# Optimization experiments

Measured on AMD Instinct MI355X. Metric: run time of the kernel, lower is better.

The kernel has to match this reference:

```python
import jax, jax.numpy as jnp
import numpy as np
import math

NUM_HEADS = 8
LN_EPS = 1e-8


def setup_inputs() -> dict:
    key = jax.random.key(0)
    ks = jax.random.split(key, 8)
    B, S, D = 16, 1024, 1024
    s = 1.0 / math.sqrt(D)
    return {
        "queries": jax.random.normal(ks[0], (B, S, D), dtype=jnp.float32),
        "keys": jax.random.normal(ks[1], (B, S, D), dtype=jnp.float32),
        "Wq": jax.random.normal(ks[2], (D, D), dtype=jnp.float32) * s,
        "bq": jnp.zeros((D,), dtype=jnp.float32),
        "Wk": jax.random.normal(ks[3], (D, D), dtype=jnp.float32) * s,
        "bk": jnp.zeros((D,), dtype=jnp.float32),
        "Wv": jax.random.normal(ks[4], (D, D), dtype=jnp.float32) * s,
        "bv": jnp.zeros((D,), dtype=jnp.float32),
        "ln_gamma": jnp.ones((D,), dtype=jnp.float32),
        "ln_beta": jnp.zeros((D,), dtype=jnp.float32),
    }


def _split_heads(x, H):
    # [B, S, D] -> [B*H, S, D/H], batch-major flattening (b*H + h), matching torch
    B, S, D = x.shape
    d = D // H
    return x.reshape(B, S, H, d).transpose(0, 2, 1, 3).reshape(B * H, S, d)


def _merge_heads(x, B, H):
    # [B*H, S, d] -> [B, S, H*d]
    BH, S, d = x.shape
    return x.reshape(B, H, S, d).transpose(0, 2, 1, 3).reshape(B, S, H * d)


def reference(queries, keys, Wq, bq, Wk, bk, Wv, bv, ln_gamma, ln_beta):
    B, S, D = queries.shape
    K_len = keys.shape[1]
    H = NUM_HEADS

    # ReLU'd QKV projections (nn.Linear uses x @ W.T + b)
    Q = jax.nn.relu(jnp.einsum("bsd,ed->bse", queries, Wq) + bq)
    K = jax.nn.relu(jnp.einsum("bsd,ed->bse", keys, Wk) + bk)
    V = jax.nn.relu(jnp.einsum("bsd,ed->bse", keys, Wv) + bv)

    Q_ = _split_heads(Q, H)  # [B*H, S, d]
    K_ = _split_heads(K, H)
    V_ = _split_heads(V, H)
    d_k = K_.shape[-1]

    scores = jnp.einsum("nsd,ntd->nst", Q_, K_) / jnp.sqrt(jnp.float32(d_k))
    attn = jax.nn.softmax(scores, axis=-1)  # [B*H, S, K_len]

    # post-softmax multiplicative mask: mask of nonzero query rows, tiled
    # head-major (mask.repeat(H,1,1)) exactly as the torch code does
    mask = (jnp.sum(jnp.abs(queries), axis=-1, keepdims=True) > 0).astype(queries.dtype)  # [B, S, 1]
    mask = jnp.broadcast_to(mask, (B, S, K_len))
    mask = jnp.tile(mask, (H, 1, 1))  # [H*B, S, K_len], index i -> batch i % B
    attn = attn * mask
    # dropout is identity in eval mode

    out = jnp.einsum("nst,ntd->nsd", attn, V_)  # [B*H, S, d]
    out = _merge_heads(out, B, H)  # [B, S, D]
    out = out + queries

    # LayerNorm over last dim, eps=1e-8
    mu = jnp.mean(out, axis=-1, keepdims=True)
    var = jnp.mean(jnp.square(out - mu), axis=-1, keepdims=True)
    out = (out - mu) / jnp.sqrt(var + LN_EPS) * ln_gamma + ln_beta
    return out
```

## Files before the change

### kernel.cpp

```cpp
#include <hip/hip_runtime.h>
#include <hip/hip_bf16.h>

#define B_ 16
#define S_ 1024
#define D_ 1024
#define H_ 8

typedef __attribute__((ext_vector_type(4))) float f32x4;
typedef __attribute__((ext_vector_type(8))) short s16x8;
typedef __attribute__((ext_vector_type(4))) short s16x4;
typedef unsigned int u32;

static __device__ __forceinline__ short f2bf(float x) {
  union { __hip_bfloat16 h; short s; } cv;
  cv.h = __float2bfloat16(x);
  return cv.s;
}
static __device__ __forceinline__ float bf2f(short x) {
  union { float f; u32 u; } cv;
  cv.u = ((u32)(unsigned short)x) << 16;
  return cv.f;
}
static __device__ __forceinline__ float exp2_hw(float x) {
  float r;
  asm("v_exp_f32 %0, %1" : "=v"(r) : "v"(x));
  return r;
}
static __device__ __forceinline__ void async16(const void* g, void* l) {
  __builtin_amdgcn_global_load_lds((const __attribute__((address_space(1))) u32*)g,
                                   (__attribute__((address_space(3))) u32*)l, 16, 0, 0);
}

#define QSCALE 0.12751741530f

__global__ __launch_bounds__(256) void cvt_qk(const float* __restrict__ q,
                                              const float* __restrict__ k,
                                              short* __restrict__ qb,
                                              short* __restrict__ kb) {
  int i = blockIdx.x * 256 + threadIdx.x;
  const float* s;
  short* d;
  int j;
  if (i < 2097152) { s = q; d = qb; j = i; }
  else             { s = k; d = kb; j = i - 2097152; }
  const float4* s4 = (const float4*)s;
  float4 a = s4[2 * j], b = s4[2 * j + 1];
  s16x8 r;
  r[0] = f2bf(a.x); r[1] = f2bf(a.y); r[2] = f2bf(a.z); r[3] = f2bf(a.w);
  r[4] = f2bf(b.x); r[5] = f2bf(b.y); r[6] = f2bf(b.z); r[7] = f2bf(b.w);
  *(s16x8*)(d + (size_t)j * 8) = r;
}

__global__ __launch_bounds__(256) void cvt_w(const float* __restrict__ wq,
                                             const float* __restrict__ wk,
                                             const float* __restrict__ wv,
                                             short* __restrict__ dq,
                                             short* __restrict__ dk,
                                             short* __restrict__ dv) {
  int i = blockIdx.x * 256 + threadIdx.x;
  const float* s;
  short* d;
  int j;
  if (i < 131072)      { s = wq; d = dq; j = i; }
  else if (i < 262144) { s = wk; d = dk; j = i - 131072; }
  else                 { s = wv; d = dv; j = i - 262144; }
  const float4* s4 = (const float4*)s;
  float4 a = s4[2 * j], b = s4[2 * j + 1];
  s16x8 r;
  r[0] = f2bf(a.x); r[1] = f2bf(a.y); r[2] = f2bf(a.z); r[3] = f2bf(a.w);
  r[4] = f2bf(b.x); r[5] = f2bf(b.y); r[6] = f2bf(b.z); r[7] = f2bf(b.w);
  *(s16x8*)(d + (size_t)j * 8) = r;
}

__global__ __launch_bounds__(256, 2) void gemm_qkv(
    const short* __restrict__ qb, const short* __restrict__ kb,
    const short* __restrict__ wq, const short* __restrict__ wk,
    const short* __restrict__ wv, const float* __restrict__ bq,
    const float* __restrict__ bk, const float* __restrict__ bv,
    short* __restrict__ Qb, short* __restrict__ Kb, short* __restrict__ Vb) {
  __shared__ short lA[128 * 64];
  __shared__ short lB[128 * 64];
  const short* A; const short* W; const float* bias; short* C;
  float scl;
  switch (blockIdx.z) {
    case 0:  A = qb; W = wq; bias = bq; C = Qb; scl = QSCALE; break;
    case 1:  A = kb; W = wk; bias = bk; C = Kb; scl = 1.f; break;
    default: A = kb; W = wv; bias = bv; C = Vb; scl = 1.f; break;
  }
  const int t = threadIdx.x;
  const int w = t >> 6, l = t & 63, lg = l >> 4, li = l & 15;
  const int wr = w >> 1, wc = w & 1;
  const int m0 = blockIdx.y << 7, n0 = blockIdx.x << 7;

  f32x4 acc[4][4];
#pragma unroll
  for (int m = 0; m < 4; ++m)
#pragma unroll
    for (int n = 0; n < 4; ++n) acc[m][n] = {0.f, 0.f, 0.f, 0.f};

  const char* Ab = (const char*)A + (size_t)m0 * 2048;
  const char* Wb = (const char*)W + (size_t)n0 * 2048;

#pragma unroll 1
  for (int k0 = 0; k0 < 1024; k0 += 64) {
    __syncthreads();
#pragma unroll
    for (int it = 0; it < 4; ++it) {
      int e = it * 256 + t;
      int row = e >> 3;
      int sb = ((e & 7) << 4) ^ ((row & 7) << 4);
      async16(Ab + (size_t)row * 2048 + k0 * 2 + sb, (char*)lA + e * 16);
      async16(Wb + (size_t)row * 2048 + k0 * 2 + sb, (char*)lB + e * 16);
    }
    __syncthreads();
#pragma unroll
    for (int kk = 0; kk < 2; ++kk) {
      s16x8 af[4], bfr[4];
#pragma unroll
      for (int m = 0; m < 4; ++m) {
        int row = wr * 64 + m * 16 + li;
        af[m] = *(const s16x8*)((char*)lA + row * 128 +
                                ((kk * 64 + (lg << 4)) ^ ((row & 7) << 4)));
      }
#pragma unroll
      for (int n = 0; n < 4; ++n) {
        int row = wc * 64 + n * 16 + li;
        bfr[n] = *(const s16x8*)((char*)lB + row * 128 +
                                 ((kk * 64 + (lg << 4)) ^ ((row & 7) << 4)));
      }
#pragma unroll
      for (int m = 0; m < 4; ++m)
#pragma unroll
        for (int n = 0; n < 4; ++n)
          acc[m][n] = __builtin_amdgcn_mfma_f32_16x16x32_bf16(af[m], bfr[n],
                                                              acc[m][n], 0, 0, 0);
    }
  }
#pragma unroll
  for (int n = 0; n < 4; ++n) {
    int col = n0 + wc * 64 + n * 16 + li;
    float bb = bias[col];
#pragma unroll
    for (int m = 0; m < 4; ++m) {
      int row0 = m0 + wr * 64 + m * 16 + (lg << 2);
#pragma unroll
      for (int r = 0; r < 4; ++r) {
        float v = acc[m][n][r] + bb;
        v = (v > 0.f ? v : 0.f) * scl;
        C[(size_t)(row0 + r) * 1024 + col] = f2bf(v);
      }
    }
  }
}

__global__ __launch_bounds__(256, 2) void attn_kernel(
    const short* __restrict__ Qb, const short* __restrict__ Kb,
    const short* __restrict__ Vb, short* __restrict__ Ob) {
  __shared__ short lK[64 * 128];
  __shared__ short lV[128 * 88];
  __shared__ short lP[128 * 64];

  const int t = threadIdx.x;
  const int w = t >> 6, l = t & 63, lg = l >> 4, li = l & 15;
  const int wgid = blockIdx.x;
  const int bh = ((wgid & 7) << 4) + (wgid >> 6);
  const int q0 = ((wgid >> 3) & 7) << 7;
  const int b = bh >> 3, h = bh & 7;
  const size_t hbase = (size_t)b * (S_ * D_) + h * 128;
  const short* Kh = Kb + hbase;
  const short* Vh = Vb + hbase;

  s16x8 qf[2][4];
#pragma unroll
  for (int m = 0; m < 2; ++m)
#pragma unroll
    for (int kk = 0; kk < 4; ++kk) {
      int row = q0 + (w << 5) + m * 16 + li;
      qf[m][kk] = *(const s16x8*)(Qb + hbase + (size_t)row * D_ + kk * 32 + (lg << 3));
    }

  f32x4 o[2][8];
#pragma unroll
  for (int m = 0; m < 2; ++m)
#pragma unroll
    for (int nd = 0; nd < 8; ++nd) o[m][nd] = {0.f, 0.f, 0.f, 0.f};
  float mrow[2][4], lrow[2][4];
#pragma unroll
  for (int m = 0; m < 2; ++m)
#pragma unroll
    for (int r = 0; r < 4; ++r) { mrow[m][r] = -1e30f; lrow[m][r] = 0.f; }

  s16x8 kreg[4], vr0[2], vr1[2];
#define LOADT(KT)                                                              \
  {                                                                            \
    _Pragma("unroll") for (int it = 0; it < 4; ++it) {                         \
      int e = it * 256 + t;                                                    \
      kreg[it] = *(const s16x8*)(Kh + (size_t)((KT)*64 + (e >> 4)) * 1024 +    \
                                 (e & 15) * 8);                                \
    }                                                                          \
    _Pragma("unroll") for (int vit = 0; vit < 2; ++vit) {                      \
      int e2 = vit * 256 + t;                                                  \
      int k0 = (e2 & 31) * 2, d0 = (e2 >> 5) * 8;                              \
      vr0[vit] = *(const s16x8*)(Vh + (size_t)((KT)*64 + k0) * 1024 + d0);     \
      vr1[vit] = *(const s16x8*)(Vh + (size_t)((KT)*64 + k0 + 1) * 1024 + d0); \
    }                                                                          \
  }

  LOADT(0);

#pragma unroll 1
  for (int kt = 0; kt < 16; ++kt) {
    __syncthreads();
#pragma unroll
    for (int it = 0; it < 4; ++it) {
      int e = it * 256 + t;
      int kr = e >> 4, kc = e & 15;
      *(s16x8*)((char*)lK + kr * 256 + ((kc * 16) ^ ((kr & 7) << 4))) = kreg[it];
    }
#pragma unroll
    for (int vit = 0; vit < 2; ++vit) {
      int e2 = vit * 256 + t;
      int k0 = (e2 & 31) * 2, d0 = (e2 >> 5) * 8;
#pragma unroll
      for (int j = 0; j < 8; ++j) {
        u32 pk = (u32)(unsigned short)vr0[vit][j] |
                 ((u32)(unsigned short)vr1[vit][j] << 16);
        *(u32*)((char*)lV + (d0 + j) * 176 + k0 * 2) = pk;
      }
    }
    __syncthreads();
    if (kt < 15) LOADT(kt + 1);

    f32x4 sc[2][4];
#pragma unroll
    for (int m = 0; m < 2; ++m)
#pragma unroll
      for (int n = 0; n < 4; ++n) sc[m][n] = {0.f, 0.f, 0.f, 0.f};
#pragma unroll
    for (int kk = 0; kk < 4; ++kk)
#pragma unroll
      for (int n = 0; n < 4; ++n) {
        int krow = n * 16 + li;
        s16x8 kf = *(const s16x8*)((char*)lK + krow * 256 +
                                   ((kk * 64 + (lg << 4)) ^ ((krow & 7) << 4)));
        sc[0][n] = __builtin_amdgcn_mfma_f32_16x16x32_bf16(qf[0][kk], kf, sc[0][n], 0, 0, 0);
        sc[1][n] = __builtin_amdgcn_mfma_f32_16x16x32_bf16(qf[1][kk], kf, sc[1][n], 0, 0, 0);
      }

    float tm[2][4];
    bool skip = true;
#pragma unroll
    for (int m = 0; m < 2; ++m)
#pragma unroll
      for (int r = 0; r < 4; ++r) {
        float v = fmaxf(fmaxf(sc[m][0][r], sc[m][1][r]),
                        fmaxf(sc[m][2][r], sc[m][3][r]));
        v = fmaxf(v, __shfl_xor(v, 1));
        v = fmaxf(v, __shfl_xor(v, 2));
        v = fmaxf(v, __shfl_xor(v, 4));
        v = fmaxf(v, __shfl_xor(v, 8));
        tm[m][r] = v;
        skip = skip && (v <= mrow[m][r] + 11.5f);
      }
    if (!__all(skip)) {
#pragma unroll
      for (int m = 0; m < 2; ++m)
#pragma unroll
        for (int r = 0; r < 4; ++r) {
          float mnew = fmaxf(mrow[m][r], tm[m][r]);
          float fsc = exp2_hw(mrow[m][r] - mnew);
          mrow[m][r] = mnew;
          lrow[m][r] *= fsc;
#pragma unroll
          for (int nd = 0; nd < 8; ++nd) o[m][nd][r] *= fsc;
        }
    }
#pragma unroll
    for (int m = 0; m < 2; ++m)
#pragma unroll
      for (int r = 0; r < 4; ++r) {
        float ps = 0.f;
#pragma unroll
        for (int n = 0; n < 4; ++n) {
          float p = exp2_hw(sc[m][n][r] - mrow[m][r]);
          sc[m][n][r] = p;
          ps += p;
        }
        ps += __shfl_xor(ps, 1);
        ps += __shfl_xor(ps, 2);
        ps += __shfl_xor(ps, 4);
        ps += __shfl_xor(ps, 8);
        lrow[m][r] += ps;
      }

#pragma unroll
    for (int m = 0; m < 2; ++m)
#pragma unroll
      for (int n = 0; n < 4; ++n)
#pragma unroll
        for (int r = 0; r < 4; ++r) {
          int prow = (w << 5) + m * 16 + (lg << 2) + r;
          int cb = ((n * 16 + li) << 1) ^ ((prow & 7) << 4);
          *(short*)((char*)lP + prow * 128 + cb) = f2bf(sc[m][n][r]);
        }
    asm volatile("s_waitcnt lgkmcnt(0)" ::: "memory");
    __builtin_amdgcn_sched_barrier(0);

#pragma unroll
    for (int ks = 0; ks < 2; ++ks) {
      int prow0 = (w << 5) + li;
      int prow1 = prow0 + 16;
      int kb3 = ks * 64 + (lg << 4);
      s16x8 pf0 = *(const s16x8*)((char*)lP + prow0 * 128 + (kb3 ^ ((prow0 & 7) << 4)));
      s16x8 pf1 = *(const s16x8*)((char*)lP + prow1 * 128 + (kb3 ^ ((prow1 & 7) << 4)));
#pragma unroll
      for (int nd = 0; nd < 8; ++nd) {
        int d = nd * 16 + li;
        s16x8 vf = *(const s16x8*)((char*)lV + d * 176 + kb3);
        o[0][nd] = __builtin_amdgcn_mfma_f32_16x16x32_bf16(pf0, vf, o[0][nd], 0, 0, 0);
        o[1][nd] = __builtin_amdgcn_mfma_f32_16x16x32_bf16(pf1, vf, o[1][nd], 0, 0, 0);
      }
    }
  }
#undef LOADT

#pragma unroll
  for (int m = 0; m < 2; ++m)
#pragma unroll
    for (int r = 0; r < 4; ++r) {
      float inv = 1.f / lrow[m][r];
      int row = q0 + (w << 5) + m * 16 + (lg << 2) + r;
      short* orow = Ob + hbase + (size_t)row * D_;
#pragma unroll
      for (int nd = 0; nd < 8; ++nd)
        orow[nd * 16 + li] = f2bf(o[m][nd][r] * inv);
    }
}

__global__ __launch_bounds__(256) void ln_ep(const float* __restrict__ q,
                                             const short* __restrict__ Ob,
                                             const float* __restrict__ gam,
                                             const float* __restrict__ bet,
                                             float* __restrict__ out) {
  __shared__ float red[4][8];
  const int t = threadIdx.x;
  const int w = t >> 6, l = t & 63;
  const size_t off = (size_t)blockIdx.x * 1024 + t * 4;
  float4 qv = *(const float4*)(q + off);
  s16x4 ov = *(const s16x4*)(Ob + off);
  float oa[4] = {bf2f(ov[0]), bf2f(ov[1]), bf2f(ov[2]), bf2f(ov[3])};
  float qa[4] = {qv.x, qv.y, qv.z, qv.w};
  float s0 = 0, s1 = 0, s2 = 0, s3 = 0, s4 = 0, s5 = 0;
#pragma unroll
  for (int j = 0; j < 4; ++j) {
    s0 += fabsf(qa[j]);
    s1 += oa[j];
    s2 += qa[j];
    s3 += oa[j] * oa[j];
    s4 += oa[j] * qa[j];
    s5 += qa[j] * qa[j];
  }
#pragma unroll
  for (int d2 = 1; d2 < 64; d2 <<= 1) {
    s0 += __shfl_xor(s0, d2); s1 += __shfl_xor(s1, d2); s2 += __shfl_xor(s2, d2);
    s3 += __shfl_xor(s3, d2); s4 += __shfl_xor(s4, d2); s5 += __shfl_xor(s5, d2);
  }
  if (l == 0) {
    red[w][0] = s0; red[w][1] = s1; red[w][2] = s2;
    red[w][3] = s3; red[w][4] = s4; red[w][5] = s5;
  }
  __syncthreads();
  s0 = red[0][0] + red[1][0] + red[2][0] + red[3][0];
  s1 = red[0][1] + red[1][1] + red[2][1] + red[3][1];
  s2 = red[0][2] + red[1][2] + red[2][2] + red[3][2];
  s3 = red[0][3] + red[1][3] + red[2][3] + red[3][3];
  s4 = red[0][4] + red[1][4] + red[2][4] + red[3][4];
  s5 = red[0][5] + red[1][5] + red[2][5] + red[3][5];
  float msk = s0 > 0.f ? 1.f : 0.f;
  float sy = msk * s1 + s2;
  float sy2 = msk * s3 + 2.f * msk * s4 + s5;
  float mean = sy * (1.f / 1024.f);
  float var = sy2 * (1.f / 1024.f) - mean * mean;
  float inv = rsqrtf(fmaxf(var, 0.f) + 1e-8f);
  float4 gv = *(const float4*)(gam + t * 4);
  float4 bv = *(const float4*)(bet + t * 4);
  float4 rr;
  rr.x = (msk * oa[0] + qa[0] - mean) * inv * gv.x + bv.x;
  rr.y = (msk * oa[1] + qa[1] - mean) * inv * gv.y + bv.y;
  rr.z = (msk * oa[2] + qa[2] - mean) * inv * gv.z + bv.z;
  rr.w = (msk * oa[3] + qa[3] - mean) * inv * gv.w + bv.w;
  *(float4*)(out + off) = rr;
}

extern "C" void kernel_launch(void* const* d_in, const int* in_sizes, int n_in,
                              void* d_out, int out_size, void* d_ws, size_t ws_size,
                              hipStream_t stream) {
  const float* q   = (const float*)d_in[0];
  const float* k   = (const float*)d_in[1];
  const float* Wq  = (const float*)d_in[2];
  const float* bq  = (const float*)d_in[3];
  const float* Wk  = (const float*)d_in[4];
  const float* bk  = (const float*)d_in[5];
  const float* Wv  = (const float*)d_in[6];
  const float* bv  = (const float*)d_in[7];
  const float* gam = (const float*)d_in[8];
  const float* bet = (const float*)d_in[9];
  float* out = (float*)d_out;

  short* qb  = (short*)d_ws;
  short* kb  = qb + 16777216;
  short* wqb = kb + 16777216;
  short* wkb = wqb + 1048576;
  short* wvb = wkb + 1048576;
  short* Qb  = wvb + 1048576;
  short* Kb  = Qb + 16777216;
  short* Vb  = Kb + 16777216;
  short* Ob  = qb;

  cvt_qk<<<16384, 256, 0, stream>>>(q, k, qb, kb);
  cvt_w<<<1536, 256, 0, stream>>>(Wq, Wk, Wv, wqb, wkb, wvb);
  gemm_qkv<<<dim3(8, 128, 3), 256, 0, stream>>>(qb, kb, wqb, wkb, wvb,
                                                bq, bk, bv, Qb, Kb, Vb);
  attn_kernel<<<1024, 256, 0, stream>>>(Qb, Kb, Vb, Ob);
  ln_ep<<<16384, 256, 0, stream>>>(q, Ob, gam, bet, out);
}
```

Before: 486.2 us.

## Rewrite QKV GEMM as 256x256 tile with double-buffered async pipeline

```diff
diff --git a/kernel.cpp b/kernel.cpp
--- a/kernel.cpp
+++ b/kernel.cpp
@@ -72,14 +72,13 @@
   *(s16x8*)(d + (size_t)j * 8) = r;
 }
 
-__global__ __launch_bounds__(256, 2) void gemm_qkv(
+__global__ __launch_bounds__(512, 1) void gemm_qkv(
     const short* __restrict__ qb, const short* __restrict__ kb,
     const short* __restrict__ wq, const short* __restrict__ wk,
     const short* __restrict__ wv, const float* __restrict__ bq,
     const float* __restrict__ bk, const float* __restrict__ bv,
     short* __restrict__ Qb, short* __restrict__ Kb, short* __restrict__ Vb) {
-  __shared__ short lA[128 * 64];
-  __shared__ short lB[128 * 64];
+  __shared__ short LDS[65536];
   const short* A; const short* W; const float* bias; short* C;
   float scl;
   switch (blockIdx.z) {
@@ -89,60 +88,118 @@
   }
   const int t = threadIdx.x;
   const int w = t >> 6, l = t & 63, lg = l >> 4, li = l & 15;
-  const int wr = w >> 1, wc = w & 1;
-  const int m0 = blockIdx.y << 7, n0 = blockIdx.x << 7;
-
-  f32x4 acc[4][4];
-#pragma unroll
-  for (int m = 0; m < 4; ++m)
+  const int wr = w >> 2, wc = w & 3;
+  const int swz = ((blockIdx.x & 7) << 5) + (blockIdx.x >> 3);
+  const int m0 = (swz >> 2) << 8;
+  const int n0 = (swz & 3) << 8;
+
+  f32x4 acc[8][4];
+#pragma unroll
+  for (int m = 0; m < 8; ++m)
 #pragma unroll
     for (int n = 0; n < 4; ++n) acc[m][n] = {0.f, 0.f, 0.f, 0.f};
 
-  const char* Ab = (const char*)A + (size_t)m0 * 2048;
-  const char* Wb = (const char*)W + (size_t)n0 * 2048;
+  auto STAGE = [&](int kt, int buf, int op, int kk) {
+    const short* src = op ? W : A;
+    const int rb = op ? n0 : m0;
+    char* dst = (char*)LDS + ((((buf << 1) | op) << 1) | kk) * 16384;
+#pragma unroll
+    for (int j = 0; j < 2; ++j) {
+      int e = j * 512 + t;
+      int row = e >> 2, ch = e & 3;
+      size_t sb = (size_t)(rb + row) * 2048 + kt * 128 + kk * 64 +
+                  ((ch ^ (row & 3)) << 4);
+      async16((const char*)src + sb, dst + e * 16);
+    }
+  };
+  const int swzRD = (lg << 4);
+  auto RDA = [&](int buf, int kk, int m) -> s16x8 {
+    int row = wr * 128 + m * 16 + li;
+    const char* p = (char*)LDS + ((((buf << 1) | 0) << 1) | kk) * 16384 +
+                    row * 64 + (swzRD ^ ((li & 3) << 4));
+    return *(const s16x8*)p;
+  };
+  auto RDB = [&](int buf, int kk, int n) -> s16x8 {
+    int row = wc * 64 + n * 16 + li;
+    const char* p = (char*)LDS + ((((buf << 1) | 1) << 1) | kk) * 16384 +
+                    row * 64 + (swzRD ^ ((li & 3) << 4));
+    return *(const s16x8*)p;
+  };
+
+  s16x8 bf0, bf1, bf2, bf3;
+
+#define MFMA16(MOFF)                                                           \
+  {                                                                            \
+    _Pragma("unroll") for (int mm = 0; mm < 4; ++mm) {                         \
+      acc[(MOFF) + mm][0] = __builtin_amdgcn_mfma_f32_16x16x32_bf16(           \
+          af[mm], bf0, acc[(MOFF) + mm][0], 0, 0, 0);                          \
+      acc[(MOFF) + mm][1] = __builtin_amdgcn_mfma_f32_16x16x32_bf16(           \
+          af[mm], bf1, acc[(MOFF) + mm][1], 0, 0, 0);                          \
+      acc[(MOFF) + mm][2] = __builtin_amdgcn_mfma_f32_16x16x32_bf16(           \
+          af[mm], bf2, acc[(MOFF) + mm][2], 0, 0, 0);                          \
+      acc[(MOFF) + mm][3] = __builtin_amdgcn_mfma_f32_16x16x32_bf16(           \
+          af[mm], bf3, acc[(MOFF) + mm][3], 0, 0, 0);                          \
+    }                                                                          \
+  }
+
+#define PHASE(CBUF, CKK, MOFF, ODDP, DOSTAGE, SKT, SBUF, SOP, SKK, WAITN)      \
+  {                                                                            \
+    s16x8 af[4];                                                               \
+    _Pragma("unroll") for (int mm = 0; mm < 4; ++mm)                           \
+        af[mm] = RDA(CBUF, CKK, (MOFF) + mm);                                  \
+    if (ODDP) {                                                                \
+      bf0 = RDB(CBUF, CKK, 0); bf1 = RDB(CBUF, CKK, 1);                        \
+      bf2 = RDB(CBUF, CKK, 2); bf3 = RDB(CBUF, CKK, 3);                        \
+    }                                                                          \
+    if (DOSTAGE) STAGE(SKT, SBUF, SOP, SKK);                                   \
+    if ((WAITN) == 8) asm volatile("s_waitcnt vmcnt(8)" ::: "memory");         \
+    if ((WAITN) == 4) asm volatile("s_waitcnt vmcnt(4)" ::: "memory");         \
+    if ((WAITN) == 0) asm volatile("s_waitcnt vmcnt(0)" ::: "memory");         \
+    __builtin_amdgcn_s_barrier();                                              \
+    asm volatile("s_waitcnt lgkmcnt(0)" ::: "memory");                         \
+    __builtin_amdgcn_sched_barrier(0);                                         \
+    __builtin_amdgcn_s_setprio(1);                                             \
+    MFMA16(MOFF);                                                              \
+    __builtin_amdgcn_s_setprio(0);                                             \
+    __builtin_amdgcn_s_barrier();                                              \
+  }
+
+  STAGE(0, 0, 0, 0); STAGE(0, 0, 1, 0);
+  STAGE(0, 0, 0, 1); STAGE(0, 0, 1, 1);
+  STAGE(1, 1, 0, 0); STAGE(1, 1, 1, 0);
+  asm volatile("s_waitcnt vmcnt(8)" ::: "memory");
+  __builtin_amdgcn_s_barrier();
 
 #pragma unroll 1
-  for (int k0 = 0; k0 < 1024; k0 += 64) {
-    __syncthreads();
-#pragma unroll
-    for (int it = 0; it < 4; ++it) {
-      int e = it * 256 + t;
-      int row = e >> 3;
-      int sb = ((e & 7) << 4) ^ ((row & 7) << 4);
-      async16(Ab + (size_t)row * 2048 + k0 * 2 + sb, (char*)lA + e * 16);
-      async16(Wb + (size_t)row * 2048 + k0 * 2 + sb, (char*)lB + e * 16);
-    }
-    __syncthreads();
-#pragma unroll
-    for (int kk = 0; kk < 2; ++kk) {
-      s16x8 af[4], bfr[4];
-#pragma unroll
-      for (int m = 0; m < 4; ++m) {
-        int row = wr * 64 + m * 16 + li;
-        af[m] = *(const s16x8*)((char*)lA + row * 128 +
-                                ((kk * 64 + (lg << 4)) ^ ((row & 7) << 4)));
-      }
-#pragma unroll
-      for (int n = 0; n < 4; ++n) {
-        int row = wc * 64 + n * 16 + li;
-        bfr[n] = *(const s16x8*)((char*)lB + row * 128 +
-                                 ((kk * 64 + (lg << 4)) ^ ((row & 7) << 4)));
-      }
-#pragma unroll
-      for (int m = 0; m < 4; ++m)
-#pragma unroll
-        for (int n = 0; n < 4; ++n)
-          acc[m][n] = __builtin_amdgcn_mfma_f32_16x16x32_bf16(af[m], bfr[n],
-                                                              acc[m][n], 0, 0, 0);
-    }
-  }
+  for (int j = 0; j < 7; ++j) {
+    const int k1 = 2 * j + 1, k2 = 2 * j + 2, k3 = 2 * j + 3;
+    PHASE(0, 0, 0, 1, 1, k1, 1, 0, 1, -1)
+    PHASE(0, 0, 4, 0, 1, k1, 1, 1, 1, 8)
+    PHASE(0, 1, 0, 1, 1, k2, 0, 0, 0, -1)
+    PHASE(0, 1, 4, 0, 1, k2, 0, 1, 0, 8)
+    PHASE(1, 0, 0, 1, 1, k2, 0, 0, 1, -1)
+    PHASE(1, 0, 4, 0, 1, k2, 0, 1, 1, 8)
+    PHASE(1, 1, 0, 1, 1, k3, 1, 0, 0, -1)
+    PHASE(1, 1, 4, 0, 1, k3, 1, 1, 0, 8)
+  }
+  PHASE(0, 0, 0, 1, 1, 15, 1, 0, 1, -1)
+  PHASE(0, 0, 4, 0, 1, 15, 1, 1, 1, 8)
+  PHASE(0, 1, 0, 1, 0, 0, 0, 0, 0, -1)
+  PHASE(0, 1, 4, 0, 0, 0, 0, 0, 0, 4)
+  PHASE(1, 0, 0, 1, 0, 0, 0, 0, 0, -1)
+  PHASE(1, 0, 4, 0, 0, 0, 0, 0, 0, 0)
+  PHASE(1, 1, 0, 1, 0, 0, 0, 0, 0, -1)
+  PHASE(1, 1, 4, 0, 0, 0, 0, 0, 0, -1)
+#undef PHASE
+#undef MFMA16
+
 #pragma unroll
   for (int n = 0; n < 4; ++n) {
     int col = n0 + wc * 64 + n * 16 + li;
     float bb = bias[col];
 #pragma unroll
-    for (int m = 0; m < 4; ++m) {
-      int row0 = m0 + wr * 64 + m * 16 + (lg << 2);
+    for (int m = 0; m < 8; ++m) {
+      int row0 = m0 + wr * 128 + m * 16 + (lg << 2);
 #pragma unroll
       for (int r = 0; r < 4; ++r) {
         float v = acc[m][n][r] + bb;
@@ -419,7 +476,7 @@
 
   cvt_qk<<<16384, 256, 0, stream>>>(q, k, qb, kb);
   cvt_w<<<1536, 256, 0, stream>>>(Wq, Wk, Wv, wqb, wkb, wvb);
-  gemm_qkv<<<dim3(8, 128, 3), 256, 0, stream>>>(qb, kb, wqb, wkb, wvb,
+  gemm_qkv<<<dim3(256, 1, 3), 512, 0, stream>>>(qb, kb, wqb, wkb, wvb,
                                                 bq, bk, bv, Qb, Kb, Vb);
   attn_kernel<<<1024, 256, 0, stream>>>(Qb, Kb, Vb, Ob);
   ln_ep<<<16384, 256, 0, stream>>>(q, Ob, gam, bet, out);
```

Measured after the change: 464.4 us. 4.5% less time.
